# Performance work log

Measured on AMD Instinct MI355X. Metric: run time of the kernel, lower is better.

## Reference

```python
import jax, jax.numpy as jnp
import numpy as np
import math

ALPHA, BETA = 0.0, 0.1  # MarketRelation defaults


def setup_inputs() -> dict:
    key = jax.random.key(0)
    ks = jax.random.split(key, 15)
    n, T, d, K, C = 1024, 8, 64, 8, 64
    h = d  # hidden = (2*infeat)//2 = infeat
    s = 0.1
    u = jax.random.uniform(ks[13], (n, n, K), jnp.float32, 1e-6, 1.0 - 1e-6)
    return {
        "x":   jax.random.normal(ks[0], (n, T, d), jnp.float32),
        "Ind": jax.random.uniform(ks[1], (n, n), jnp.float32),
        "Loc": jax.random.uniform(ks[2], (n, n), jnp.float32),
        "a":   jax.random.normal(ks[3], (T, 1), jnp.float32),
        "W1m": jax.random.normal(ks[4], (2 * d, h), jnp.float32) * s,
        "b1m": jax.random.normal(ks[5], (h,), jnp.float32) * s,
        "W2m": jax.random.normal(ks[6], (h, 1), jnp.float32) * s,
        "b2m": jax.random.normal(ks[7], (1,), jnp.float32) * s,
        "W1s": jax.random.normal(ks[8], (2 * d, h), jnp.float32) * s,
        "b1s": jax.random.normal(ks[9], (h,), jnp.float32) * s,
        "W2s": jax.random.normal(ks[10], (h, K), jnp.float32) * s,
        "b2s": jax.random.normal(ks[11], (K,), jnp.float32) * s,
        "E":   jax.random.normal(ks[12], (K, n, C), jnp.float32) * s,
        "g":   -jnp.log(-jnp.log(u)),  # Gumbel(0,1) noise for gumbel_softmax
    }


def reference(x, Ind, Loc, a, W1m, b1m, W2m, b2m, W1s, b1s, W2s, b2s, E, g):
    n, T, d = x.shape
    # --- MarketRelation ---
    # fc1(concat(x_j, x_k)) == x_j @ W1m[:d] + x_k @ W1m[d:] + b1m (same math,
    # avoids materializing the N x N x 2d concat tensor)
    W1a, W1b = W1m[:d], W1m[d:]
    a_soft = jax.nn.softmax(a, axis=0)  # [T,1]
    A_mkt = jnp.zeros((n, n), x.dtype)
    for i in range(T):
        xi = x[:, i, :]                      # [n,d]
        hA = xi @ W1a                        # [n,h]
        hB = xi @ W1b                        # [n,h]
        hmat = jax.nn.relu(hA[:, None, :] + hB[None, :, :] + b1m)  # [n,n,h]
        adj = jax.nn.relu(hmat @ W2m + b2m)[..., 0]                # [n,n]
        factor = 1.0 + ALPHA * math.exp(-BETA * (T - i - 1))
        A_mkt = A_mkt + adj * (a_soft[i, 0] * factor)
    # --- NobsRelation (on last timestep) ---
    xl = x[:, -1, :]
    Ws1a, Ws1b = W1s[:d], W1s[d:]
    hs = jax.nn.relu((xl @ Ws1a)[:, None, :] + (xl @ Ws1b)[None, :, :] + b1s)
    logits = jax.nn.relu(hs @ W2s + b2s)          # [n,n,K]
    y = jax.nn.softmax(logits + g, axis=-1)       # gumbel_softmax, tau=1, soft
    D = jnp.einsum('knc,kmc->nmk', E, E)          # stack of E_k E_k^T, [n,n,K]
    A_nobs = jnp.sum(D * y, axis=-1)              # [n,n]
    return jnp.stack([Ind, Loc, A_mkt, A_nobs])   # [4,n,n]
```

## Files before the change

kernel.cpp:

```cpp
#include <hip/hip_runtime.h>

typedef unsigned short USH;
typedef unsigned int UIN;
typedef _Float16 F16;
typedef F16 h2 __attribute__((ext_vector_type(2)));
typedef short bfrag __attribute__((ext_vector_type(8)));
typedef float f32x4 __attribute__((ext_vector_type(4)));

__device__ __forceinline__ float bf2f(USH u) {
    return __uint_as_float(((unsigned int)u) << 16);
}
__device__ __forceinline__ USH f2bf(float f) {
    unsigned int i = __float_as_uint(f);
    i += 0x7FFFu + ((i >> 16) & 1u);
    return (USH)(i >> 16);
}
__device__ __forceinline__ UIN pkh2(float a, float b) {
    h2 h; h.x = (F16)a; h.y = (F16)b;
    return __builtin_bit_cast(UIN, h);
}
__device__ __forceinline__ h2 u2h(UIN u) { return __builtin_bit_cast(h2, u); }
__device__ __forceinline__ h2 relu2h(h2 s) {
    const h2 zz = {(F16)0.0f, (F16)0.0f};
    return __builtin_elementwise_max(s, zz);
}
__device__ __forceinline__ float fdot2(h2 a, h2 b, float c) {
#if __has_builtin(__builtin_amdgcn_fdot2)
    return __builtin_amdgcn_fdot2(a, b, c, false);
#else
    return c + (float)a.x * (float)b.x + (float)a.y * (float)b.y;
#endif
}

__device__ __forceinline__ float ldf(const void* p, long idx, int bf) {
    return bf ? bf2f(((const USH*)p)[idx]) : ((const float*)p)[idx];
}
__device__ __forceinline__ void ld4(const void* p, long idx, int bf, float o[4]) {
    if (bf) {
        ushort4 u = *(const ushort4*)((const USH*)p + idx);
        o[0] = bf2f(u.x); o[1] = bf2f(u.y); o[2] = bf2f(u.z); o[3] = bf2f(u.w);
    } else {
        float4 v = *(const float4*)((const float*)p + idx);
        o[0] = v.x; o[1] = v.y; o[2] = v.z; o[3] = v.w;
    }
}

__device__ __forceinline__ int detect_bf(const void* ind) {
    const uint4* p = (const uint4*)ind;
    unsigned o = 0;
    #pragma unroll
    for (int i = 0; i < 8; ++i) { uint4 v = p[i]; o |= v.x | v.y | v.z | v.w; }
    return (o & 0x8000u) == 0;
}


__global__ __launch_bounds__(256) void k_pre_d(
    const void* __restrict__ x,
    const void* __restrict__ W1m,
    const void* __restrict__ b1m,
    const void* __restrict__ W1s,
    const void* __restrict__ b1s,
    const void* __restrict__ E,
    const void* __restrict__ IndDet,
    UIN* __restrict__ hA16,
    UIN* __restrict__ hB16,
    USH* __restrict__ D)
{
    __shared__ float smem[8192];
    const int bf = detect_bf(IndDet);
    const int tid = threadIdx.x;
    const int bid = blockIdx.x;

    if (bid < 512) {
        USH* sE = (USH*)smem;
        const int k = bid >> 6;
        const int nb = ((bid >> 3) & 7) * 128, mb = (bid & 7) * 128;
        const long ek = (long)k * 65536;

        const int row = tid >> 1;
        const int c0 = (tid & 1) * 32;
        #pragma unroll
        for (int side = 0; side < 2; ++side) {
            const int rbase = side ? mb : nb;
            USH* sDst = sE + side * 8192;
            const long gbase = ek + (long)(rbase + row) * 64 + c0;
            USH tmp[32];
            if (bf) {
                #pragma unroll
                for (int q = 0; q < 4; ++q)
                    *(uint4*)&tmp[q * 8] = *(const uint4*)((const USH*)E + gbase + q * 8);
            } else {
                #pragma unroll
                for (int q = 0; q < 4; ++q) {
                    const float4 va = *(const float4*)((const float*)E + gbase + q * 8);
                    const float4 vb = *(const float4*)((const float*)E + gbase + q * 8 + 4);
                    tmp[q * 8 + 0] = f2bf(va.x); tmp[q * 8 + 1] = f2bf(va.y);
                    tmp[q * 8 + 2] = f2bf(va.z); tmp[q * 8 + 3] = f2bf(va.w);
                    tmp[q * 8 + 4] = f2bf(vb.x); tmp[q * 8 + 5] = f2bf(vb.y);
                    tmp[q * 8 + 6] = f2bf(vb.z); tmp[q * 8 + 7] = f2bf(vb.w);
                }
            }
            #pragma unroll
            for (int q = 0; q < 4; ++q) {
                const int byte = (c0 + q * 8) * 2;
                const int sw = (row * 128 + (byte ^ ((row & 7) << 4))) >> 1;
                *(uint4*)&sDst[sw] = *(uint4*)&tmp[q * 8];
            }
        }
        __syncthreads();

        const int lane = tid & 63;
        const int w = tid >> 6;
        const int wn = (w >> 1) * 64, wm = (w & 1) * 64;
        const int fr = lane & 15, kg = lane >> 4;

        f32x4 acc[4][4] = {};
        #pragma unroll
        for (int ks = 0; ks < 2; ++ks) {
            const int cb = (ks * 32 + kg * 8) * 2;
            bfrag af[4], bfv[4];
            #pragma unroll
            for (int f = 0; f < 4; ++f) {
                const int ra = wn + f * 16 + fr;
                af[f] = *(const bfrag*)&sE[(ra * 128 + (cb ^ ((ra & 7) << 4))) >> 1];
                const int rb = wm + f * 16 + fr;
                bfv[f] = *(const bfrag*)&sE[8192 + ((rb * 128 + (cb ^ ((rb & 7) << 4))) >> 1)];
            }
            #pragma unroll
            for (int fn = 0; fn < 4; ++fn)
                #pragma unroll
                for (int fm = 0; fm < 4; ++fm)
                    acc[fn][fm] = __builtin_amdgcn_mfma_f32_16x16x32_bf16(
                        af[fn], bfv[fm], acc[fn][fm], 0, 0, 0);
        }

        USH* Dk = D + ((long)k << 20);
        #pragma unroll
        for (int fn = 0; fn < 4; ++fn) {
            const int nrow = nb + wn + fn * 16 + kg * 4;
            #pragma unroll
            for (int fm = 0; fm < 4; ++fm) {
                const int mcol = mb + wm + fm * 16 + fr;
                #pragma unroll
                for (int r = 0; r < 4; ++r)
                    Dk[(long)(nrow + r) * 1024 + mcol] = f2bf(acc[fn][fm][r]);
            }
        }
    } else {
        float* sA = smem;
        float* sB = smem + 4096;
        const int tx = tid & 15, ty = tid >> 4;
        const int bid2 = bid - 512;
        const int nbase = (bid2 & 15) * 64;
        const int by = bid2 >> 4;
        int t, rb;
        const void* Wsrc;
        const void* bias;
        UIN* dst;
        if (by < 8)        { t = by;     rb = 0;  Wsrc = W1m; bias = nullptr; dst = hA16 + by * 32768; }
        else if (by < 16)  { t = by - 8; rb = 64; Wsrc = W1m; bias = b1m;     dst = hB16 + (by - 8) * 32768; }
        else if (by == 16) { t = 7;      rb = 0;  Wsrc = W1s; bias = nullptr; dst = hA16 + 8 * 32768; }
        else               { t = 7;      rb = 64; Wsrc = W1s; bias = b1s;     dst = hB16 + 8 * 32768; }

        {
            const int n_l = tid >> 2, dq = tid & 3;
            const long base = (long)(nbase + n_l) * 512 + t * 64 + dq * 16;
            #pragma unroll
            for (int j = 0; j < 4; ++j) {
                float o[4]; ld4(x, base + j * 4, bf, o);
                const int d0 = dq * 16 + j * 4;
                #pragma unroll
                for (int e = 0; e < 4; ++e) sA[(d0 + e) * 64 + n_l] = o[e];
            }
        }
        {
            const int d_l = tid >> 2, cq = tid & 3;
            const long base = (long)(rb + d_l) * 64 + cq * 16;
            #pragma unroll
            for (int j = 0; j < 4; ++j) {
                float o[4]; ld4(Wsrc, base + j * 4, bf, o);
                const int c0 = cq * 16 + j * 4;
                #pragma unroll
                for (int e = 0; e < 4; ++e) sB[d_l * 64 + c0 + e] = o[e];
            }
        }
        __syncthreads();

        const int c0 = tx * 4, nq = ty * 4;
        float acc[4][4] = {};
        #pragma unroll 16
        for (int d = 0; d < 64; ++d) {
            const float4 xa = *(const float4*)&sA[d * 64 + nq];
            const float4 wv = *(const float4*)&sB[d * 64 + c0];
            const float aa[4] = {xa.x, xa.y, xa.z, xa.w};
            const float ww[4] = {wv.x, wv.y, wv.z, wv.w};
            #pragma unroll
            for (int ci = 0; ci < 4; ++ci)
                #pragma unroll
                for (int ni = 0; ni < 4; ++ni)
                    acc[ci][ni] += ww[ci] * aa[ni];
        }
        float b[4] = {0.f, 0.f, 0.f, 0.f};
        if (bias) {
            #pragma unroll
            for (int ci = 0; ci < 4; ++ci) b[ci] = ldf(bias, c0 + ci, bf);
        }
        const int cp0 = c0 >> 1;
        #pragma unroll
        for (int ni = 0; ni < 4; ++ni) {
            const int col = nbase + nq + ni;
            dst[cp0 * 1024 + col]       = pkh2(acc[0][ni] + b[0], acc[1][ni] + b[1]);
            dst[(cp0 + 1) * 1024 + col] = pkh2(acc[2][ni] + b[2], acc[3][ni] + b[3]);
        }
    }
}

__global__ __launch_bounds__(64) void k_main(
    const UIN* __restrict__ hA16,
    const UIN* __restrict__ hB16,
    const USH* __restrict__ Dm,
    const void* __restrict__ Ind, const void* __restrict__ Loc,
    const void* __restrict__ a, const void* __restrict__ W2m,
    const void* __restrict__ b2m, const void* __restrict__ W2s,
    const void* __restrict__ b2s, const void* __restrict__ g,
    void* __restrict__ out)
{
    __shared__ UIN As[512];
    __shared__ UIN Bs[512];
    __shared__ UIN w2m16[32];
    __shared__ UIN w2s16[256];
    __shared__ float asoft_l[8];

    const int bf = detect_bf(Ind);
    const int tid = threadIdx.x;
    const int mb = blockIdx.x * 16, nb = blockIdx.y * 16;
    const int m0 = (tid & 7) * 2;
    const int n0 = (tid >> 3) * 2;

    if (tid < 32) w2m16[tid] = pkh2(ldf(W2m, 2 * tid, bf), ldf(W2m, 2 * tid + 1, bf));
    {
        const int cp = tid >> 1, kh = (tid & 1) * 4;
        #pragma unroll
        for (int e = 0; e < 4; ++e) {
            const int k = kh + e;
            w2s16[cp * 8 + k] = pkh2(ldf(W2s, (2 * cp) * 8 + k, bf),
                                     ldf(W2s, (2 * cp + 1) * 8 + k, bf));
        }
    }
    if (tid < 8) {
        float av[8], mx = -1e30f, s = 0.0f;
        #pragma unroll
        for (int k = 0; k < 8; ++k) { av[k] = ldf(a, k, bf); mx = fmaxf(mx, av[k]); }
        #pragma unroll
        for (int k = 0; k < 8; ++k) s += __expf(av[k] - mx);
        asoft_l[tid] = __expf(av[tid] - mx) / s;
    }
    const float b2m_f = ldf(b2m, 0, bf);

    const int cpS = tid >> 1, half = tid & 1;
    const int offA = cpS * 1024 + nb + half * 8;
    const int offB = cpS * 1024 + mb + half * 8;
    const int ldsS = cpS * 16 + half * 8;

    {
        const uint4 a0 = *(const uint4*)(hA16 + offA);
        const uint4 a1 = *(const uint4*)(hA16 + offA + 4);
        const uint4 b0 = *(const uint4*)(hB16 + offB);
        const uint4 b1 = *(const uint4*)(hB16 + offB + 4);
        *(uint4*)&As[ldsS] = a0; *(uint4*)&As[ldsS + 4] = a1;
        *(uint4*)&Bs[ldsS] = b0; *(uint4*)&Bs[ldsS + 4] = b1;
    }

    float amk[2][2] = {{0.f, 0.f}, {0.f, 0.f}};

    for (int t = 0; t < 8; ++t) {
        const uint4 pa0 = *(const uint4*)(hA16 + (t + 1) * 32768 + offA);
        const uint4 pa1 = *(const uint4*)(hA16 + (t + 1) * 32768 + offA + 4);
        const uint4 pb0 = *(const uint4*)(hB16 + (t + 1) * 32768 + offB);
        const uint4 pb1 = *(const uint4*)(hB16 + (t + 1) * 32768 + offB + 4);

        float a00 = 0.f, a01 = 0.f, a10 = 0.f, a11 = 0.f;
        #pragma unroll
        for (int cp = 0; cp < 32; ++cp) {
            const uint2 au = *(const uint2*)&As[(cp << 4) + n0];
            const uint2 bu = *(const uint2*)&Bs[(cp << 4) + m0];
            const h2 wv = u2h(w2m16[cp]);
            const h2 a0 = u2h(au.x), a1 = u2h(au.y);
            const h2 b0 = u2h(bu.x), b1 = u2h(bu.y);
            const h2 z00 = relu2h(a0 + b0), z01 = relu2h(a0 + b1);
            const h2 z10 = relu2h(a1 + b0), z11 = relu2h(a1 + b1);
            a00 = fdot2(z00, wv, a00); a01 = fdot2(z01, wv, a01);
            a10 = fdot2(z10, wv, a10); a11 = fdot2(z11, wv, a11);
        }
        const float as_t = asoft_l[t];
        amk[0][0] += fmaxf(a00 + b2m_f, 0.f) * as_t;
        amk[0][1] += fmaxf(a01 + b2m_f, 0.f) * as_t;
        amk[1][0] += fmaxf(a10 + b2m_f, 0.f) * as_t;
        amk[1][1] += fmaxf(a11 + b2m_f, 0.f) * as_t;

        *(uint4*)&As[ldsS] = pa0; *(uint4*)&As[ldsS + 4] = pa1;
        *(uint4*)&Bs[ldsS] = pb0; *(uint4*)&Bs[ldsS + 4] = pb1;
    }

    float lg[2][2][8];
    #pragma unroll
    for (int i = 0; i < 2; ++i)
        #pragma unroll
        for (int j = 0; j < 2; ++j)
            #pragma unroll
            for (int k = 0; k < 8; ++k) lg[i][j][k] = 0.f;

    #pragma unroll 8
    for (int cp = 0; cp < 32; ++cp) {
        const uint2 au = *(const uint2*)&As[(cp << 4) + n0];
        const uint2 bu = *(const uint2*)&Bs[(cp << 4) + m0];
        const h2 a0 = u2h(au.x), a1 = u2h(au.y);
        const h2 b0 = u2h(bu.x), b1 = u2h(bu.y);
        const h2 z00 = relu2h(a0 + b0), z01 = relu2h(a0 + b1);
        const h2 z10 = relu2h(a1 + b0), z11 = relu2h(a1 + b1);
        const uint4 wa = *(const uint4*)&w2s16[cp * 8];
        const uint4 wb = *(const uint4*)&w2s16[cp * 8 + 4];
        const UIN wks[8] = {wa.x, wa.y, wa.z, wa.w, wb.x, wb.y, wb.z, wb.w};
        #pragma unroll
        for (int k = 0; k < 8; ++k) {
            const h2 wv = u2h(wks[k]);
            lg[0][0][k] = fdot2(z00, wv, lg[0][0][k]);
            lg[0][1][k] = fdot2(z01, wv, lg[0][1][k]);
            lg[1][0][k] = fdot2(z10, wv, lg[1][0][k]);
            lg[1][1][k] = fdot2(z11, wv, lg[1][1][k]);
        }
    }

    float b2s_f[8];
    #pragma unroll
    for (int k = 0; k < 8; ++k) b2s_f[k] = ldf(b2s, k, bf);

    #pragma unroll
    for (int i = 0; i < 2; ++i) {
        const long rowoff = (long)(nb + n0 + i) * 1024 + mb + m0;
        float gv[16];
        ld4(g, rowoff * 8 + 0, bf, gv + 0);
        ld4(g, rowoff * 8 + 4, bf, gv + 4);
        ld4(g, rowoff * 8 + 8, bf, gv + 8);
        ld4(g, rowoff * 8 + 12, bf, gv + 12);

        float s0 = 0.0f, s1 = 0.0f, d0 = 0.0f, d1 = 0.0f;
        #pragma unroll
        for (int k = 0; k < 8; ++k) {
            const float l0 = fmaxf(lg[i][0][k] + b2s_f[k], 0.f);
            const float l1 = fmaxf(lg[i][1][k] + b2s_f[k], 0.f);
            const float e0 = __expf(l0 + gv[k]);
            const float e1 = __expf(l1 + gv[8 + k]);
            s0 += e0; s1 += e1;
            const ushort2 dv = *(const ushort2*)&Dm[((long)k << 20) + rowoff];
            d0 += bf2f(dv.x) * e0;
            d1 += bf2f(dv.y) * e1;
        }

        if (bf) {
            USH* o = (USH*)out;
            *(ushort2*)&o[rowoff] = *(const ushort2*)&((const USH*)Ind)[rowoff];
            *(ushort2*)&o[1048576 + rowoff] = *(const ushort2*)&((const USH*)Loc)[rowoff];
            ushort2 o2; o2.x = f2bf(amk[i][0]); o2.y = f2bf(amk[i][1]);
            *(ushort2*)&o[2 * 1048576 + rowoff] = o2;
            ushort2 o3; o3.x = f2bf(d0 / s0); o3.y = f2bf(d1 / s1);
            *(ushort2*)&o[3 * 1048576 + rowoff] = o3;
        } else {
            float* o = (float*)out;
            *(float2*)&o[rowoff] = *(const float2*)&((const float*)Ind)[rowoff];
            *(float2*)&o[1048576 + rowoff] = *(const float2*)&((const float*)Loc)[rowoff];
            float2 o2; o2.x = amk[i][0]; o2.y = amk[i][1];
            *(float2*)&o[2 * 1048576 + rowoff] = o2;
            float2 o3; o3.x = d0 / s0; o3.y = d1 / s1;
            *(float2*)&o[3 * 1048576 + rowoff] = o3;
        }
    }
}

extern "C" void kernel_launch(void* const* d_in, const int* in_sizes, int n_in,
                              void* d_out, int out_size, void* d_ws, size_t ws_size,
                              hipStream_t stream) {
    const void* x   = d_in[0];
    const void* Ind = d_in[1];
    const void* Loc = d_in[2];
    const void* a   = d_in[3];
    const void* W1m = d_in[4];
    const void* b1m = d_in[5];
    const void* W2m = d_in[6];
    const void* b2m = d_in[7];
    const void* W1s = d_in[8];
    const void* b1s = d_in[9];
    const void* W2s = d_in[10];
    const void* b2s = d_in[11];
    const void* E   = d_in[12];
    const void* g   = d_in[13];

    UIN* ws   = (UIN*)d_ws;
    UIN* hA16 = ws;
    UIN* hB16 = hA16 + 294912;
    USH* Dm   = (USH*)(hB16 + 294912);

    k_pre_d<<<dim3(800), 256, 0, stream>>>(x, W1m, b1m, W1s, b1s, E, Ind,
                                           hA16, hB16, Dm);
    k_main<<<dim3(64, 64), 64, 0, stream>>>(hA16, hB16, Dm,
                                            Ind, Loc, a, W2m, b2m, W2s, b2s,
                                            g, d_out);
}
```

Measured before the change: 167.3 us.

## Fuse E_k E_k^T computation into main kernel via per-tile MFMA

Stops writing the full K×n×n bf16 D tensor (16 MB) in the precompute kernel; each 16x16 output tile in the main kernel now computes its D_k block on the fly with two bf16 MFMAs per k, reading E directly. The thread mapping changes from 2x2 to 1x4 per thread to match the MFMA output fragment layout, so the gumbel-softmax weights line up with accumulator rows. This removes a large global write and read at the cost of redundant E loads and MFMA work per tile, plus narrower scalar output stores.

```diff
diff --git a/kernel.cpp b/kernel.cpp
--- a/kernel.cpp
+++ b/kernel.cpp
@@ -44,6 +44,20 @@
         o[0] = v.x; o[1] = v.y; o[2] = v.z; o[3] = v.w;
     }
 }
+__device__ __forceinline__ bfrag ldfragE(const void* E, long idx, int bf) {
+    if (bf) {
+        return __builtin_bit_cast(bfrag, *(const uint4*)((const USH*)E + idx));
+    } else {
+        const float4 va = *(const float4*)((const float*)E + idx);
+        const float4 vb = *(const float4*)((const float*)E + idx + 4);
+        bfrag r;
+        r[0] = (short)f2bf(va.x); r[1] = (short)f2bf(va.y);
+        r[2] = (short)f2bf(va.z); r[3] = (short)f2bf(va.w);
+        r[4] = (short)f2bf(vb.x); r[5] = (short)f2bf(vb.y);
+        r[6] = (short)f2bf(vb.z); r[7] = (short)f2bf(vb.w);
+        return r;
+    }
+}
 
 __device__ __forceinline__ int detect_bf(const void* ind) {
     const uint4* p = (const uint4*)ind;
@@ -60,165 +74,84 @@
     const void* __restrict__ b1m,
     const void* __restrict__ W1s,
     const void* __restrict__ b1s,
-    const void* __restrict__ E,
     const void* __restrict__ IndDet,
     UIN* __restrict__ hA16,
-    UIN* __restrict__ hB16,
-    USH* __restrict__ D)
+    UIN* __restrict__ hB16)
 {
     __shared__ float smem[8192];
+    float* sA = smem;
+    float* sB = smem + 4096;
     const int bf = detect_bf(IndDet);
     const int tid = threadIdx.x;
     const int bid = blockIdx.x;
-
-    if (bid < 512) {
-        USH* sE = (USH*)smem;
-        const int k = bid >> 6;
-        const int nb = ((bid >> 3) & 7) * 128, mb = (bid & 7) * 128;
-        const long ek = (long)k * 65536;
-
-        const int row = tid >> 1;
-        const int c0 = (tid & 1) * 32;
-        #pragma unroll
-        for (int side = 0; side < 2; ++side) {
-            const int rbase = side ? mb : nb;
-            USH* sDst = sE + side * 8192;
-            const long gbase = ek + (long)(rbase + row) * 64 + c0;
-            USH tmp[32];
-            if (bf) {
-                #pragma unroll
-                for (int q = 0; q < 4; ++q)
-                    *(uint4*)&tmp[q * 8] = *(const uint4*)((const USH*)E + gbase + q * 8);
-            } else {
-                #pragma unroll
-                for (int q = 0; q < 4; ++q) {
-                    const float4 va = *(const float4*)((const float*)E + gbase + q * 8);
-                    const float4 vb = *(const float4*)((const float*)E + gbase + q * 8 + 4);
-                    tmp[q * 8 + 0] = f2bf(va.x); tmp[q * 8 + 1] = f2bf(va.y);
-                    tmp[q * 8 + 2] = f2bf(va.z); tmp[q * 8 + 3] = f2bf(va.w);
-                    tmp[q * 8 + 4] = f2bf(vb.x); tmp[q * 8 + 5] = f2bf(vb.y);
-                    tmp[q * 8 + 6] = f2bf(vb.z); tmp[q * 8 + 7] = f2bf(vb.w);
-                }
-            }
+    const int tx = tid & 15, ty = tid >> 4;
+    const int nbase = (bid & 15) * 64;
+    const int by = bid >> 4;
+    int t, rb;
+    const void* Wsrc;
+    const void* bias;
+    UIN* dst;
+    if (by < 8)        { t = by;     rb = 0;  Wsrc = W1m; bias = nullptr; dst = hA16 + by * 32768; }
+    else if (by < 16)  { t = by - 8; rb = 64; Wsrc = W1m; bias = b1m;     dst = hB16 + (by - 8) * 32768; }
+    else if (by == 16) { t = 7;      rb = 0;  Wsrc = W1s; bias = nullptr; dst = hA16 + 8 * 32768; }
+    else               { t = 7;      rb = 64; Wsrc = W1s; bias = b1s;     dst = hB16 + 8 * 32768; }
+
+    {
+        const int n_l = tid >> 2, dq = tid & 3;
+        const long base = (long)(nbase + n_l) * 512 + t * 64 + dq * 16;
+        #pragma unroll
+        for (int j = 0; j < 4; ++j) {
+            float o[4]; ld4(x, base + j * 4, bf, o);
+            const int d0 = dq * 16 + j * 4;
             #pragma unroll
-            for (int q = 0; q < 4; ++q) {
-                const int byte = (c0 + q * 8) * 2;
-                const int sw = (row * 128 + (byte ^ ((row & 7) << 4))) >> 1;
-                *(uint4*)&sDst[sw] = *(uint4*)&tmp[q * 8];
-            }
-        }
-        __syncthreads();
-
-        const int lane = tid & 63;
-        const int w = tid >> 6;
-        const int wn = (w >> 1) * 64, wm = (w & 1) * 64;
-        const int fr = lane & 15, kg = lane >> 4;
-
-        f32x4 acc[4][4] = {};
-        #pragma unroll
-        for (int ks = 0; ks < 2; ++ks) {
-            const int cb = (ks * 32 + kg * 8) * 2;
-            bfrag af[4], bfv[4];
+            for (int e = 0; e < 4; ++e) sA[(d0 + e) * 64 + n_l] = o[e];
+        }
+    }
+    {
+        const int d_l = tid >> 2, cq = tid & 3;
+        const long base = (long)(rb + d_l) * 64 + cq * 16;
+        #pragma unroll
+        for (int j = 0; j < 4; ++j) {
+            float o[4]; ld4(Wsrc, base + j * 4, bf, o);
+            const int c0 = cq * 16 + j * 4;
             #pragma unroll
-            for (int f = 0; f < 4; ++f) {
-                const int ra = wn + f * 16 + fr;
-                af[f] = *(const bfrag*)&sE[(ra * 128 + (cb ^ ((ra & 7) << 4))) >> 1];
-                const int rb = wm + f * 16 + fr;
-                bfv[f] = *(const bfrag*)&sE[8192 + ((rb * 128 + (cb ^ ((rb & 7) << 4))) >> 1)];
-            }
+            for (int e = 0; e < 4; ++e) sB[d_l * 64 + c0 + e] = o[e];
+        }
+    }
+    __syncthreads();
+
+    const int c0 = tx * 4, nq = ty * 4;
+    float acc[4][4] = {};
+    #pragma unroll 16
+    for (int d = 0; d < 64; ++d) {
+        const float4 xa = *(const float4*)&sA[d * 64 + nq];
+        const float4 wv = *(const float4*)&sB[d * 64 + c0];
+        const float aa[4] = {xa.x, xa.y, xa.z, xa.w};
+        const float ww[4] = {wv.x, wv.y, wv.z, wv.w};
+        #pragma unroll
+        for (int ci = 0; ci < 4; ++ci)
             #pragma unroll
-            for (int fn = 0; fn < 4; ++fn)
-                #pragma unroll
-                for (int fm = 0; fm < 4; ++fm)
-                    acc[fn][fm] = __builtin_amdgcn_mfma_f32_16x16x32_bf16(
-                        af[fn], bfv[fm], acc[fn][fm], 0, 0, 0);
-        }
-
-        USH* Dk = D + ((long)k << 20);
-        #pragma unroll
-        for (int fn = 0; fn < 4; ++fn) {
-            const int nrow = nb + wn + fn * 16 + kg * 4;
-            #pragma unroll
-            for (int fm = 0; fm < 4; ++fm) {
-                const int mcol = mb + wm + fm * 16 + fr;
-                #pragma unroll
-                for (int r = 0; r < 4; ++r)
-                    Dk[(long)(nrow + r) * 1024 + mcol] = f2bf(acc[fn][fm][r]);
-            }
-        }
-    } else {
-        float* sA = smem;
-        float* sB = smem + 4096;
-        const int tx = tid & 15, ty = tid >> 4;
-        const int bid2 = bid - 512;
-        const int nbase = (bid2 & 15) * 64;
-        const int by = bid2 >> 4;
-        int t, rb;
-        const void* Wsrc;
-        const void* bias;
-        UIN* dst;
-        if (by < 8)        { t = by;     rb = 0;  Wsrc = W1m; bias = nullptr; dst = hA16 + by * 32768; }
-        else if (by < 16)  { t = by - 8; rb = 64; Wsrc = W1m; bias = b1m;     dst = hB16 + (by - 8) * 32768; }
-        else if (by == 16) { t = 7;      rb = 0;  Wsrc = W1s; bias = nullptr; dst = hA16 + 8 * 32768; }
-        else               { t = 7;      rb = 64; Wsrc = W1s; bias = b1s;     dst = hB16 + 8 * 32768; }
-
-        {
-            const int n_l = tid >> 2, dq = tid & 3;
-            const long base = (long)(nbase + n_l) * 512 + t * 64 + dq * 16;
-            #pragma unroll
-            for (int j = 0; j < 4; ++j) {
-                float o[4]; ld4(x, base + j * 4, bf, o);
-                const int d0 = dq * 16 + j * 4;
-                #pragma unroll
-                for (int e = 0; e < 4; ++e) sA[(d0 + e) * 64 + n_l] = o[e];
-            }
-        }
-        {
-            const int d_l = tid >> 2, cq = tid & 3;
-            const long base = (long)(rb + d_l) * 64 + cq * 16;
-            #pragma unroll
-            for (int j = 0; j < 4; ++j) {
-                float o[4]; ld4(Wsrc, base + j * 4, bf, o);
-                const int c0 = cq * 16 + j * 4;
-                #pragma unroll
-                for (int e = 0; e < 4; ++e) sB[d_l * 64 + c0 + e] = o[e];
-            }
-        }
-        __syncthreads();
-
-        const int c0 = tx * 4, nq = ty * 4;
-        float acc[4][4] = {};
-        #pragma unroll 16
-        for (int d = 0; d < 64; ++d) {
-            const float4 xa = *(const float4*)&sA[d * 64 + nq];
-            const float4 wv = *(const float4*)&sB[d * 64 + c0];
-            const float aa[4] = {xa.x, xa.y, xa.z, xa.w};
-            const float ww[4] = {wv.x, wv.y, wv.z, wv.w};
-            #pragma unroll
-            for (int ci = 0; ci < 4; ++ci)
-                #pragma unroll
-                for (int ni = 0; ni < 4; ++ni)
-                    acc[ci][ni] += ww[ci] * aa[ni];
-        }
-        float b[4] = {0.f, 0.f, 0.f, 0.f};
-        if (bias) {
-            #pragma unroll
-            for (int ci = 0; ci < 4; ++ci) b[ci] = ldf(bias, c0 + ci, bf);
-        }
-        const int cp0 = c0 >> 1;
-        #pragma unroll
-        for (int ni = 0; ni < 4; ++ni) {
-            const int col = nbase + nq + ni;
-            dst[cp0 * 1024 + col]       = pkh2(acc[0][ni] + b[0], acc[1][ni] + b[1]);
-            dst[(cp0 + 1) * 1024 + col] = pkh2(acc[2][ni] + b[2], acc[3][ni] + b[3]);
-        }
+            for (int ni = 0; ni < 4; ++ni)
+                acc[ci][ni] += ww[ci] * aa[ni];
+    }
+    float b[4] = {0.f, 0.f, 0.f, 0.f};
+    if (bias) {
+        #pragma unroll
+        for (int ci = 0; ci < 4; ++ci) b[ci] = ldf(bias, c0 + ci, bf);
+    }
+    const int cp0 = c0 >> 1;
+    #pragma unroll
+    for (int ni = 0; ni < 4; ++ni) {
+        const int col = nbase + nq + ni;
+        dst[cp0 * 1024 + col]       = pkh2(acc[0][ni] + b[0], acc[1][ni] + b[1]);
+        dst[(cp0 + 1) * 1024 + col] = pkh2(acc[2][ni] + b[2], acc[3][ni] + b[3]);
     }
 }
 
 __global__ __launch_bounds__(64) void k_main(
     const UIN* __restrict__ hA16,
     const UIN* __restrict__ hB16,
-    const USH* __restrict__ Dm,
+    const void* __restrict__ E,
     const void* __restrict__ Ind, const void* __restrict__ Loc,
     const void* __restrict__ a, const void* __restrict__ W2m,
     const void* __restrict__ b2m, const void* __restrict__ W2s,
@@ -234,8 +167,8 @@
     const int bf = detect_bf(Ind);
     const int tid = threadIdx.x;
     const int mb = blockIdx.x * 16, nb = blockIdx.y * 16;
-    const int m0 = (tid & 7) * 2;
-    const int n0 = (tid >> 3) * 2;
+    const int m0 = tid & 15;
+    const int n0 = (tid >> 4) * 4;
 
     if (tid < 32) w2m16[tid] = pkh2(ldf(W2m, 2 * tid, bf), ldf(W2m, 2 * tid + 1, bf));
     {
@@ -271,7 +204,7 @@
         *(uint4*)&Bs[ldsS] = b0; *(uint4*)&Bs[ldsS + 4] = b1;
     }
 
-    float amk[2][2] = {{0.f, 0.f}, {0.f, 0.f}};
+    float amk[4] = {0.f, 0.f, 0.f, 0.f};
 
     for (int t = 0; t < 8; ++t) {
         const uint4 pa0 = *(const uint4*)(hA16 + (t + 1) * 32768 + offA);
@@ -279,55 +212,53 @@
         const uint4 pb0 = *(const uint4*)(hB16 + (t + 1) * 32768 + offB);
         const uint4 pb1 = *(const uint4*)(hB16 + (t + 1) * 32768 + offB + 4);
 
-        float a00 = 0.f, a01 = 0.f, a10 = 0.f, a11 = 0.f;
+        float acc[4] = {0.f, 0.f, 0.f, 0.f};
         #pragma unroll
         for (int cp = 0; cp < 32; ++cp) {
-            const uint2 au = *(const uint2*)&As[(cp << 4) + n0];
-            const uint2 bu = *(const uint2*)&Bs[(cp << 4) + m0];
+            const uint4 au = *(const uint4*)&As[(cp << 4) + n0];
+            const UIN bu = Bs[(cp << 4) + m0];
             const h2 wv = u2h(w2m16[cp]);
-            const h2 a0 = u2h(au.x), a1 = u2h(au.y);
-            const h2 b0 = u2h(bu.x), b1 = u2h(bu.y);
-            const h2 z00 = relu2h(a0 + b0), z01 = relu2h(a0 + b1);
-            const h2 z10 = relu2h(a1 + b0), z11 = relu2h(a1 + b1);
-            a00 = fdot2(z00, wv, a00); a01 = fdot2(z01, wv, a01);
-            a10 = fdot2(z10, wv, a10); a11 = fdot2(z11, wv, a11);
+            const h2 hb = u2h(bu);
+            const h2 z0 = relu2h(u2h(au.x) + hb);
+            const h2 z1 = relu2h(u2h(au.y) + hb);
+            const h2 z2 = relu2h(u2h(au.z) + hb);
+            const h2 z3 = relu2h(u2h(au.w) + hb);
+            acc[0] = fdot2(z0, wv, acc[0]);
+            acc[1] = fdot2(z1, wv, acc[1]);
+            acc[2] = fdot2(z2, wv, acc[2]);
+            acc[3] = fdot2(z3, wv, acc[3]);
         }
         const float as_t = asoft_l[t];
-        amk[0][0] += fmaxf(a00 + b2m_f, 0.f) * as_t;
-        amk[0][1] += fmaxf(a01 + b2m_f, 0.f) * as_t;
-        amk[1][0] += fmaxf(a10 + b2m_f, 0.f) * as_t;
-        amk[1][1] += fmaxf(a11 + b2m_f, 0.f) * as_t;
+        #pragma unroll
+        for (int r = 0; r < 4; ++r)
+            amk[r] += fmaxf(acc[r] + b2m_f, 0.f) * as_t;
 
         *(uint4*)&As[ldsS] = pa0; *(uint4*)&As[ldsS + 4] = pa1;
         *(uint4*)&Bs[ldsS] = pb0; *(uint4*)&Bs[ldsS + 4] = pb1;
     }
 
-    float lg[2][2][8];
-    #pragma unroll
-    for (int i = 0; i < 2; ++i)
-        #pragma unroll
-        for (int j = 0; j < 2; ++j)
-            #pragma unroll
-            for (int k = 0; k < 8; ++k) lg[i][j][k] = 0.f;
+    float lg[4][8];
+    #pragma unroll
+    for (int r = 0; r < 4; ++r)
+        #pragma unroll
+        for (int k = 0; k < 8; ++k) lg[r][k] = 0.f;
 
     #pragma unroll 8
     for (int cp = 0; cp < 32; ++cp) {
-        const uint2 au = *(const uint2*)&As[(cp << 4) + n0];
-        const uint2 bu = *(const uint2*)&Bs[(cp << 4) + m0];
-        const h2 a0 = u2h(au.x), a1 = u2h(au.y);
-        const h2 b0 = u2h(bu.x), b1 = u2h(bu.y);
-        const h2 z00 = relu2h(a0 + b0), z01 = relu2h(a0 + b1);
-        const h2 z10 = relu2h(a1 + b0), z11 = relu2h(a1 + b1);
+        const uint4 au = *(const uint4*)&As[(cp << 4) + n0];
+        const UIN bu = Bs[(cp << 4) + m0];
+        const h2 hb = u2h(bu);
+        const h2 z[4] = {relu2h(u2h(au.x) + hb), relu2h(u2h(au.y) + hb),
+                         relu2h(u2h(au.z) + hb), relu2h(u2h(au.w) + hb)};
         const uint4 wa = *(const uint4*)&w2s16[cp * 8];
         const uint4 wb = *(const uint4*)&w2s16[cp * 8 + 4];
         const UIN wks[8] = {wa.x, wa.y, wa.z, wa.w, wb.x, wb.y, wb.z, wb.w};
         #pragma unroll
         for (int k = 0; k < 8; ++k) {
             const h2 wv = u2h(wks[k]);
-            lg[0][0][k] = fdot2(z00, wv, lg[0][0][k]);
-            lg[0][1][k] = fdot2(z01, wv, lg[0][1][k]);
-            lg[1][0][k] = fdot2(z10, wv, lg[1][0][k]);
-            lg[1][1][k] = fdot2(z11, wv, lg[1][1][k]);
+            #pragma unroll
+            for (int r = 0; r < 4; ++r)
+                lg[r][k] = fdot2(z[r], wv, lg[r][k]);
         }
     }
 
@@ -335,44 +266,58 @@
     #pragma unroll
     for (int k = 0; k < 8; ++k) b2s_f[k] = ldf(b2s, k, bf);
 
-    #pragma unroll
-    for (int i = 0; i < 2; ++i) {
-        const long rowoff = (long)(nb + n0 + i) * 1024 + mb + m0;
-        float gv[16];
+    float e[4][8], sden[4];
+    #pragma unroll
+    for (int r = 0; r < 4; ++r) {
+        const long rowoff = (long)(nb + n0 + r) * 1024 + mb + m0;
+        float gv[8];
         ld4(g, rowoff * 8 + 0, bf, gv + 0);
         ld4(g, rowoff * 8 + 4, bf, gv + 4);
-        ld4(g, rowoff * 8 + 8, bf, gv + 8);
-        ld4(g, rowoff * 8 + 12, bf, gv + 12);
-
-        float s0 = 0.0f, s1 = 0.0f, d0 = 0.0f, d1 = 0.0f;
+        float s = 0.f;
         #pragma unroll
         for (int k = 0; k < 8; ++k) {
-            const float l0 = fmaxf(lg[i][0][k] + b2s_f[k], 0.f);
-            const float l1 = fmaxf(lg[i][1][k] + b2s_f[k], 0.f);
-            const float e0 = __expf(l0 + gv[k]);
-            const float e1 = __expf(l1 + gv[8 + k]);
-            s0 += e0; s1 += e1;
-            const ushort2 dv = *(const ushort2*)&Dm[((long)k << 20) + rowoff];
-            d0 += bf2f(dv.x) * e0;
-            d1 += bf2f(dv.y) * e1;
-        }
-
+            const float l = fmaxf(lg[r][k] + b2s_f[k], 0.f);
+            const float ee = __expf(l + gv[k]);
+            e[r][k] = ee; s += ee;
+        }
+        sden[r] = s;
+    }
+
+    const int fr_ = tid & 15, kg_ = tid >> 4;
+    const long an = (long)(nb + fr_) * 64 + kg_ * 8;
+    const long am = (long)(mb + fr_) * 64 + kg_ * 8;
+    float dacc[4] = {0.f, 0.f, 0.f, 0.f};
+    #pragma unroll 2
+    for (int k = 0; k < 8; ++k) {
+        const long ek = (long)k << 16;
+        const bfrag af0 = ldfragE(E, ek + an, bf);
+        const bfrag af1 = ldfragE(E, ek + an + 32, bf);
+        const bfrag bf0 = ldfragE(E, ek + am, bf);
+        const bfrag bf1 = ldfragE(E, ek + am + 32, bf);
+        f32x4 dk = {};
+        dk = __builtin_amdgcn_mfma_f32_16x16x32_bf16(af0, bf0, dk, 0, 0, 0);
+        dk = __builtin_amdgcn_mfma_f32_16x16x32_bf16(af1, bf1, dk, 0, 0, 0);
+        #pragma unroll
+        for (int r = 0; r < 4; ++r)
+            dacc[r] += dk[r] * e[r][k];
+    }
+
+    #pragma unroll
+    for (int r = 0; r < 4; ++r) {
+        const long rowoff = (long)(nb + n0 + r) * 1024 + mb + m0;
+        const float nobs = dacc[r] / sden[r];
         if (bf) {
             USH* o = (USH*)out;
-            *(ushort2*)&o[rowoff] = *(const ushort2*)&((const USH*)Ind)[rowoff];
-            *(ushort2*)&o[1048576 + rowoff] = *(const ushort2*)&((const USH*)Loc)[rowoff];
-            ushort2 o2; o2.x = f2bf(amk[i][0]); o2.y = f2bf(amk[i][1]);
-            *(ushort2*)&o[2 * 1048576 + rowoff] = o2;
-            ushort2 o3; o3.x = f2bf(d0 / s0); o3.y = f2bf(d1 / s1);
-            *(ushort2*)&o[3 * 1048576 + rowoff] = o3;
+            o[rowoff] = ((const USH*)Ind)[rowoff];
+            o[1048576 + rowoff] = ((const USH*)Loc)[rowoff];
+            o[2 * 1048576 + rowoff] = f2bf(amk[r]);
+            o[3 * 1048576 + rowoff] = f2bf(nobs);
         } else {
             float* o = (float*)out;
-            *(float2*)&o[rowoff] = *(const float2*)&((const float*)Ind)[rowoff];
-            *(float2*)&o[1048576 + rowoff] = *(const float2*)&((const float*)Loc)[rowoff];
-            float2 o2; o2.x = amk[i][0]; o2.y = amk[i][1];
-            *(float2*)&o[2 * 1048576 + rowoff] = o2;
-            float2 o3; o3.x = d0 / s0; o3.y = d1 / s1;
-            *(float2*)&o[3 * 1048576 + rowoff] = o3;
+            o[rowoff] = ((const float*)Ind)[rowoff];
+            o[1048576 + rowoff] = ((const float*)Loc)[rowoff];
+            o[2 * 1048576 + rowoff] = amk[r];
+            o[3 * 1048576 + rowoff] = nobs;
         }
     }
 }
@@ -398,11 +343,10 @@
     UIN* ws   = (UIN*)d_ws;
     UIN* hA16 = ws;
     UIN* hB16 = hA16 + 294912;
-    USH* Dm   = (USH*)(hB16 + 294912);
-
-    k_pre_d<<<dim3(800), 256, 0, stream>>>(x, W1m, b1m, W1s, b1s, E, Ind,
-                                           hA16, hB16, Dm);
-    k_main<<<dim3(64, 64), 64, 0, stream>>>(hA16, hB16, Dm,
+
+    k_pre_d<<<dim3(288), 256, 0, stream>>>(x, W1m, b1m, W1s, b1s, Ind,
+                                           hA16, hB16);
+    k_main<<<dim3(64, 64), 64, 0, stream>>>(hA16, hB16, E,
                                             Ind, Loc, a, W2m, b2m, W2s, b2s,
                                             g, d_out);
 }
```

After: 176.4 us. +5.4%, slower.
